# Optimization experiments

Hardware: AMD Instinct MI355X
Metric: run time of the kernel (lower is better)

## Reference

```python
import jax, jax.numpy as jnp
import numpy as np

RES = 8  # lattice resolution per dim (hardcoded in module)


def _neighbors():
    # 8 corner offsets of the unit cube, shape [8, 3]
    return jnp.stack(jnp.meshgrid(*([jnp.arange(2)] * 3), indexing='ij'), axis=-1).reshape(8, 3)


def _conv3d_periodic(img, kernel):
    # img: [D, H, W, Cin]; kernel: [3, 3, 3, Cout, Cin] (DHWOI layout, as in the module)
    x = jnp.pad(img, ((1, 1), (1, 1), (1, 1), (0, 0)), mode='wrap')[None]  # periodic box
    out = jax.lax.conv_general_dilated(
        x, kernel, window_strides=(1, 1, 1), padding='VALID',
        dimension_numbers=('NDHWC', 'DHWOI', 'NDHWC'))
    return out[0]


def setup_inputs() -> dict:
    key = jax.random.key(0)
    k1, k2, k3, k4, k5 = jax.random.split(key, 5)
    N, CIN, COUT, CHID = 500000, 32, 32, 32
    pos = jax.random.uniform(k1, (N, 3), dtype=jnp.float32)          # positions in [0,1)
    inp = jax.random.normal(k2, (N, CIN), dtype=jnp.float32)          # per-point features
    encoder_kernel = jax.random.normal(k3, (3, 3, 3, CHID, CIN), dtype=jnp.float32)
    inner_kernel = jax.random.normal(k4, (1, 3, 3, 3, CHID, CHID), dtype=jnp.float32)
    decoder_kernel = jax.random.normal(k5, (3, 3, 3, COUT, CHID), dtype=jnp.float32)
    return {"pos": pos, "input": inp, "encoder_kernel": encoder_kernel,
            "inner_kernel": inner_kernel, "decoder_kernel": decoder_kernel}


def reference(pos, input, encoder_kernel, inner_kernel, decoder_kernel):
    res = RES
    offsets = _neighbors()                                   # [8, 3]
    scaled = pos * res                                       # [N, 3]
    base = jnp.floor(scaled)
    frac = scaled - base                                     # trilinear fractions in [0,1)
    idxs = (base.astype(jnp.int32)[:, None, :] + offsets[None]) % res   # [N, 8, 3]
    # trilinear weights: prod over dims of frac (corner=1) or 1-frac (corner=0)
    w = jnp.where(offsets[None].astype(frac.dtype) == 1.0,
                  frac[:, None, :], 1.0 - frac[:, None, :])  # [N, 8, 3]
    weights = jnp.prod(w, axis=-1)                           # [N, 8]

    # scatter-add point features into the 8x8x8 lattice
    C = input.shape[-1]
    img = jnp.zeros((res, res, res, C), input.dtype).at[
        idxs[..., 0], idxs[..., 1], idxs[..., 2]].add(weights[..., None] * input[:, None, :])

    out = _conv3d_periodic(img, encoder_kernel)
    for k in inner_kernel:                                   # num_inner=1 residual silu blocks
        r = out
        out = r + jax.nn.silu(_conv3d_periodic(r, k))
    out = _conv3d_periodic(out, decoder_kernel)

    # gather back at the 8 corner cells (AggregationMethod.Nothing), then sum corners
    gathered = out[idxs[..., 0], idxs[..., 1], idxs[..., 2]]  # [N, 8, Cout]
    return gathered.sum(axis=1).reshape(input.shape[0], -1)
```

## Files before the change

### kernel.cpp

```cpp
#include <hip/hip_runtime.h>
#include <hip/hip_bf16.h>
#include <math.h>

#define NCELL 512
#define IMG_F 16384
#define NB    256
#define SPLIT 4

__global__ __launch_bounds__(256) void k_hist(
    const float* __restrict__ pos, int n, int* __restrict__ blockCnt)
{
    __shared__ int h[NCELL];
    const int t = threadIdx.x;
    for (int i = t; i < NCELL; i += 256) h[i] = 0;
    __syncthreads();
    const int stride = NB * 256;
    for (int p = blockIdx.x * 256 + t; p < n; p += stride) {
        const int ix = ((int)floorf(pos[3*p+0]*8.f)) & 7;
        const int iy = ((int)floorf(pos[3*p+1]*8.f)) & 7;
        const int iz = ((int)floorf(pos[3*p+2]*8.f)) & 7;
        atomicAdd(&h[ix*64 + iy*8 + iz], 1);
    }
    __syncthreads();
    for (int i = t; i < NCELL; i += 256)
        blockCnt[i * NB + blockIdx.x] = h[i];
}

__global__ __launch_bounds__(NB) void k_colscan(
    const int* __restrict__ blockCnt,
    int* __restrict__ relBase,
    int* __restrict__ cellTot)
{
    __shared__ int s[NB];
    const int cell = blockIdx.x, b = threadIdx.x;
    const int v = blockCnt[cell * NB + b];
    s[b] = v;
    __syncthreads();
    int acc = v;
    for (int off = 1; off < NB; off <<= 1) {
        const int add = (b >= off) ? s[b - off] : 0;
        __syncthreads();
        acc += add;
        s[b] = acc;
        __syncthreads();
    }
    relBase[cell * NB + b] = acc - v;
    if (b == NB - 1) cellTot[cell] = acc;
}

__global__ __launch_bounds__(NCELL) void k_scan512(
    const int* __restrict__ cellTot, int* __restrict__ binStart)
{
    __shared__ int s[NCELL];
    const int t = threadIdx.x;
    const int v = cellTot[t];
    s[t] = v;
    __syncthreads();
    int acc = v;
    for (int off = 1; off < NCELL; off <<= 1) {
        const int add = (t >= off) ? s[t - off] : 0;
        __syncthreads();
        acc += add;
        s[t] = acc;
        __syncthreads();
    }
    binStart[t] = acc - v;
    if (t == NCELL - 1) binStart[NCELL] = acc;
}

__global__ __launch_bounds__(256) void k_reorder(
    const float* __restrict__ pos, int n,
    const int* __restrict__ relBase, const int* __restrict__ binStart,
    float4* __restrict__ meta)
{
    __shared__ int cur[NCELL];
    const int t = threadIdx.x;
    for (int i = t; i < NCELL; i += 256)
        cur[i] = binStart[i] + relBase[i * NB + blockIdx.x];
    __syncthreads();
    const int stride = NB * 256;
    for (int p = blockIdx.x * 256 + t; p < n; p += stride) {
        const float sx = pos[3*p+0]*8.f, sy = pos[3*p+1]*8.f, sz = pos[3*p+2]*8.f;
        const float bx = floorf(sx), by = floorf(sy), bz = floorf(sz);
        const int ix = ((int)bx) & 7, iy = ((int)by) & 7, iz = ((int)bz) & 7;
        const int cell = ix*64 + iy*8 + iz;
        const int slot = atomicAdd(&cur[cell], 1);
        meta[slot] = make_float4(sx - bx, sy - by, sz - bz, __int_as_float(p));
    }
}

__global__ __launch_bounds__(512, 8) void k_accum(
    const float4* __restrict__ meta,
    const float* __restrict__ feat,
    const int* __restrict__ binStart,
    float* __restrict__ Mbuf)
{
    const int cell  = blockIdx.x >> 2;
    const int split = blockIdx.x & (SPLIT - 1);
    const int t = threadIdx.x;
    const int c = t & 31, sub = t >> 5;
    const int b0 = binStart[cell], cnt = binStart[cell + 1] - b0;
    const int s0 = b0 + (cnt * split) / SPLIT;
    const int s1 = b0 + (cnt * (split + 1)) / SPLIT;

    float acc[8];
    #pragma unroll
    for (int k = 0; k < 8; k++) acc[k] = 0.f;

    int i = s0 + sub;
    for (; i + 48 < s1; i += 64) {
        float4 m[4];
        float  v[4];
        #pragma unroll
        for (int j = 0; j < 4; j++) m[j] = meta[i + 16*j];
        #pragma unroll
        for (int j = 0; j < 4; j++)
            v[j] = feat[(size_t)__float_as_int(m[j].w) * 32 + c];
        #pragma unroll
        for (int j = 0; j < 4; j++) {
            const float gx = 1.f - m[j].x, gy = 1.f - m[j].y, gz = 1.f - m[j].z;
            const float a00 = gx*gy, a01 = gx*m[j].y, a10 = m[j].x*gy, a11 = m[j].x*m[j].y;
            acc[0] = fmaf(a00 * gz,     v[j], acc[0]);
            acc[1] = fmaf(a00 * m[j].z, v[j], acc[1]);
            acc[2] = fmaf(a01 * gz,     v[j], acc[2]);
            acc[3] = fmaf(a01 * m[j].z, v[j], acc[3]);
            acc[4] = fmaf(a10 * gz,     v[j], acc[4]);
            acc[5] = fmaf(a10 * m[j].z, v[j], acc[5]);
            acc[6] = fmaf(a11 * gz,     v[j], acc[6]);
            acc[7] = fmaf(a11 * m[j].z, v[j], acc[7]);
        }
    }
    for (; i < s1; i += 16) {
        const float4 m = meta[i];
        const float v = feat[(size_t)__float_as_int(m.w) * 32 + c];
        const float gx = 1.f - m.x, gy = 1.f - m.y, gz = 1.f - m.z;
        const float a00 = gx*gy, a01 = gx*m.y, a10 = m.x*gy, a11 = m.x*m.y;
        acc[0] = fmaf(a00 * gz,  v, acc[0]);
        acc[1] = fmaf(a00 * m.z, v, acc[1]);
        acc[2] = fmaf(a01 * gz,  v, acc[2]);
        acc[3] = fmaf(a01 * m.z, v, acc[3]);
        acc[4] = fmaf(a10 * gz,  v, acc[4]);
        acc[5] = fmaf(a10 * m.z, v, acc[5]);
        acc[6] = fmaf(a11 * gz,  v, acc[6]);
        acc[7] = fmaf(a11 * m.z, v, acc[7]);
    }

    __shared__ float red[16 * 8 * 32];
    #pragma unroll
    for (int k = 0; k < 8; k++) red[sub*256 + k*32 + c] = acc[k];
    __syncthreads();
    if (t < 256) {
        const int k = t >> 5, cc = t & 31;
        float s = 0.f;
        #pragma unroll
        for (int ss = 0; ss < 16; ss++) s += red[ss*256 + k*32 + cc];
        Mbuf[(blockIdx.x*8 + k)*32 + cc] = s;
    }
}

__global__ __launch_bounds__(256) void k_flush(
    const float* __restrict__ Mbuf, float* __restrict__ img)
{
    const int tid = blockIdx.x*256 + threadIdx.x;
    if (tid >= 4096) return;
    const int cell = tid >> 3, c4 = tid & 7;
    const int x = cell >> 6, y = (cell >> 3) & 7, z = cell & 7;
    const float4* M4 = (const float4*)Mbuf;
    float4 s = {0.f, 0.f, 0.f, 0.f};
    #pragma unroll
    for (int k = 0; k < 8; k++) {
        const int dx = (k >> 2) & 1, dy = (k >> 1) & 1, dz = k & 1;
        const int b = ((x - dx) & 7)*64 + ((y - dy) & 7)*8 + ((z - dz) & 7);
        #pragma unroll
        for (int sp = 0; sp < SPLIT; sp++) {
            const float4 v = M4[((b*SPLIT + sp)*8 + k)*8 + c4];
            s.x += v.x; s.y += v.y; s.z += v.z; s.w += v.w;
        }
    }
    ((float4*)img)[tid] = s;
}

template<int ACT>
__global__ __launch_bounds__(512) void k_conv(
    const float* __restrict__ in_lat,
    const float* __restrict__ w,
    float* __restrict__ out_lat)
{
    __shared__ float lds[72*36];
    __shared__ float red2[8*64];
    const int t = threadIdx.x;
    const int ixy = blockIdx.x >> 2;
    const int qq  = blockIdx.x & 3;
    const int ix = ixy >> 3, iy = ixy & 7;

    for (int i = t; i < 576; i += 512) {
        const int cellL = i >> 3, c4 = i & 7;
        const int s9 = cellL >> 3, nz = cellL & 7;
        const int jx = s9 / 3, jy = s9 - jx*3;
        const int gx = (ix + jx + 7) & 7, gy = (iy + jy + 7) & 7;
        const float4 v = ((const float4*)in_lat)[(gx*64 + gy*8 + nz)*8 + c4];
        *(float4*)&lds[cellL*36 + c4*4] = v;
    }
    __syncthreads();

    const int iz   = t & 7;
    const int co8  = (t >> 3) & 7;
    const int part = t >> 6;
    const int cout = qq*8 + co8;

    float4 acc = {0.f,0.f,0.f,0.f};
    const int tau0 = (part * 27) >> 3, tau1 = ((part + 1) * 27) >> 3;
    for (int tau = tau0; tau < tau1; ++tau) {
        const int kd = tau / 9, r = tau - kd*9;
        const int kh = r / 3,  kw = r - kh*3;
        const int nz = (iz + kw + 7) & 7;
        const float* lrow = &lds[((kd*3 + kh)*8 + nz)*36];
        const float* wrow = &w[(size_t)(tau*32 + cout)*32];
        #pragma unroll
        for (int c4i = 0; c4i < 8; c4i++) {
            const float4 a = *(const float4*)(lrow + c4i*4);
            const float4 b = *(const float4*)(wrow + c4i*4);
            acc.x = fmaf(a.x, b.x, acc.x);
            acc.y = fmaf(a.y, b.y, acc.y);
            acc.z = fmaf(a.z, b.z, acc.z);
            acc.w = fmaf(a.w, b.w, acc.w);
        }
    }
    red2[part*64 + co8*8 + iz] = (acc.x + acc.y) + (acc.z + acc.w);
    __syncthreads();

    if (t < 64) {
        const int oco8 = t >> 3, oiz = t & 7;
        float s = 0.f;
        #pragma unroll
        for (int pp = 0; pp < 8; pp++) s += red2[pp*64 + t];
        const int oidx = (ix*64 + iy*8 + oiz)*32 + qq*8 + oco8;
        if (ACT == 1) {
            const float rres = in_lat[oidx];
            s = rres + s / (1.f + expf(-s));
        }
        out_lat[oidx] = s;
    }
}

__global__ __launch_bounds__(256) void k_agg(
    const float* __restrict__ out_lat, float* __restrict__ agg)
{
    const int tid = blockIdx.x*256 + threadIdx.x;
    if (tid >= 4096) return;
    const int cell = tid >> 3, c4 = tid & 7;
    const int ix = cell >> 6, iy = (cell >> 3) & 7, iz = cell & 7;
    float4 s = {0.f,0.f,0.f,0.f};
    #pragma unroll
    for (int k = 0; k < 8; k++) {
        const int nx = (ix + ((k>>2)&1)) & 7;
        const int ny = (iy + ((k>>1)&1)) & 7;
        const int nz = (iz + (k&1)) & 7;
        const float4 v = ((const float4*)out_lat)[(nx*64 + ny*8 + nz)*8 + c4];
        s.x += v.x; s.y += v.y; s.z += v.z; s.w += v.w;
    }
    ((float4*)agg)[tid] = s;
}

__global__ __launch_bounds__(256) void k_gather(
    const float* __restrict__ pos,
    const float* __restrict__ agg,
    float* __restrict__ out,
    int n)
{
    const int tid = blockIdx.x*256 + threadIdx.x;
    const int p = tid >> 3, c4 = tid & 7;
    if (p >= n) return;
    const int ix = ((int)floorf(pos[3*p+0]*8.f)) & 7;
    const int iy = ((int)floorf(pos[3*p+1]*8.f)) & 7;
    const int iz = ((int)floorf(pos[3*p+2]*8.f)) & 7;
    ((float4*)out)[tid] = ((const float4*)agg)[(ix*64 + iy*8 + iz)*8 + c4];
}

extern "C" void kernel_launch(void* const* d_in, const int* in_sizes, int n_in,
                              void* d_out, int out_size, void* d_ws, size_t ws_size,
                              hipStream_t stream)
{
    const float* pos  = (const float*)d_in[0];
    const float* feat = (const float*)d_in[1];
    const float* wenc = (const float*)d_in[2];
    const float* winn = (const float*)d_in[3];
    const float* wdec = (const float*)d_in[4];
    float* out = (float*)d_out;
    const int n = in_sizes[0] / 3;

    float4* meta     = (float4*)d_ws;
    float*  Mbuf     = (float*)(meta + n);
    float*  img      = Mbuf + NCELL*SPLIT*8*32;
    float*  h1       = img  + IMG_F;
    float*  h2       = h1   + IMG_F;
    float*  olat     = h2   + IMG_F;
    float*  aggb     = olat + IMG_F;
    int*    blockCnt = (int*)(aggb + IMG_F);
    int*    relBase  = blockCnt + NCELL*NB;
    int*    cellTot  = relBase + NCELL*NB;
    int*    binStart = cellTot + NCELL;

    k_hist   <<<NB,    256, 0, stream>>>(pos, n, blockCnt);
    k_colscan<<<NCELL, NB,  0, stream>>>(blockCnt, relBase, cellTot);
    k_scan512<<<1,   NCELL, 0, stream>>>(cellTot, binStart);
    k_reorder<<<NB,    256, 0, stream>>>(pos, n, relBase, binStart, meta);
    k_accum  <<<NCELL*SPLIT, 512, 0, stream>>>(meta, feat, binStart, Mbuf);
    k_flush  <<<16,    256, 0, stream>>>(Mbuf, img);
    k_conv<0><<<256,   512, 0, stream>>>(img, wenc, h1);
    k_conv<1><<<256,   512, 0, stream>>>(h1,  winn, h2);
    k_conv<0><<<256,   512, 0, stream>>>(h2,  wdec, olat);
    k_agg    <<<16,    256, 0, stream>>>(olat, aggb);
    const int gblocks = (n*8 + 255)/256;
    k_gather <<<gblocks, 256, 0, stream>>>(pos, aggb, out, n);
}
```

Baseline: 177.6 us.

## Fold scan into reorder, flush into encoder conv, cache cell index for gather

The single-block 512-cell scan is merged into k_reorder: every block redundantly scans cellTot and block 0 writes binStart. The flush of the split accumulation buffer is fused into the encoder convolution's LDS fill, which removes the img buffer and one launch. k_reorder also stores a 16-bit cell index per point, so k_gather reads 2 bytes instead of 12 bytes of positions and skips the floor math. The trade-off is redundant scan work in every block, redundant flush reads in each conv block, and an extra 1 MB write in reorder.

```diff
diff --git a/kernel.cpp b/kernel.cpp
--- a/kernel.cpp
+++ b/kernel.cpp
@@ -48,44 +48,50 @@
     if (b == NB - 1) cellTot[cell] = acc;
 }
 
-__global__ __launch_bounds__(NCELL) void k_scan512(
-    const int* __restrict__ cellTot, int* __restrict__ binStart)
-{
-    __shared__ int s[NCELL];
-    const int t = threadIdx.x;
-    const int v = cellTot[t];
-    s[t] = v;
-    __syncthreads();
-    int acc = v;
-    for (int off = 1; off < NCELL; off <<= 1) {
-        const int add = (t >= off) ? s[t - off] : 0;
+__global__ __launch_bounds__(256) void k_reorder(
+    const float* __restrict__ pos, int n,
+    const int* __restrict__ relBase, const int* __restrict__ cellTot,
+    int* __restrict__ binStart,
+    float4* __restrict__ meta,
+    unsigned short* __restrict__ cellIdx)
+{
+    __shared__ int sScan[256];
+    __shared__ int cur[NCELL];
+    const int t = threadIdx.x;
+    const int bx = blockIdx.x;
+
+    const int v0 = cellTot[2*t], v1 = cellTot[2*t + 1];
+    const int ps = v0 + v1;
+    sScan[t] = ps;
+    __syncthreads();
+    int acc = ps;
+    for (int off = 1; off < 256; off <<= 1) {
+        const int add = (t >= off) ? sScan[t - off] : 0;
         __syncthreads();
         acc += add;
-        s[t] = acc;
+        sScan[t] = acc;
         __syncthreads();
     }
-    binStart[t] = acc - v;
-    if (t == NCELL - 1) binStart[NCELL] = acc;
-}
-
-__global__ __launch_bounds__(256) void k_reorder(
-    const float* __restrict__ pos, int n,
-    const int* __restrict__ relBase, const int* __restrict__ binStart,
-    float4* __restrict__ meta)
-{
-    __shared__ int cur[NCELL];
-    const int t = threadIdx.x;
-    for (int i = t; i < NCELL; i += 256)
-        cur[i] = binStart[i] + relBase[i * NB + blockIdx.x];
-    __syncthreads();
+    const int exclPair = acc - ps;
+    const int e0 = exclPair, e1 = exclPair + v0;
+    if (bx == 0) {
+        binStart[2*t]     = e0;
+        binStart[2*t + 1] = e1;
+        if (t == 255) binStart[NCELL] = acc;
+    }
+    cur[2*t]     = e0 + relBase[(2*t)     * NB + bx];
+    cur[2*t + 1] = e1 + relBase[(2*t + 1) * NB + bx];
+    __syncthreads();
+
     const int stride = NB * 256;
-    for (int p = blockIdx.x * 256 + t; p < n; p += stride) {
+    for (int p = bx * 256 + t; p < n; p += stride) {
         const float sx = pos[3*p+0]*8.f, sy = pos[3*p+1]*8.f, sz = pos[3*p+2]*8.f;
-        const float bx = floorf(sx), by = floorf(sy), bz = floorf(sz);
-        const int ix = ((int)bx) & 7, iy = ((int)by) & 7, iz = ((int)bz) & 7;
+        const float bxf = floorf(sx), byf = floorf(sy), bzf = floorf(sz);
+        const int ix = ((int)bxf) & 7, iy = ((int)byf) & 7, iz = ((int)bzf) & 7;
         const int cell = ix*64 + iy*8 + iz;
         const int slot = atomicAdd(&cur[cell], 1);
-        meta[slot] = make_float4(sx - bx, sy - by, sz - bz, __int_as_float(p));
+        meta[slot] = make_float4(sx - bxf, sy - byf, sz - bzf, __int_as_float(p));
+        cellIdx[p] = (unsigned short)cell;
     }
 }
 
@@ -158,26 +164,72 @@
     }
 }
 
-__global__ __launch_bounds__(256) void k_flush(
-    const float* __restrict__ Mbuf, float* __restrict__ img)
-{
-    const int tid = blockIdx.x*256 + threadIdx.x;
-    if (tid >= 4096) return;
-    const int cell = tid >> 3, c4 = tid & 7;
-    const int x = cell >> 6, y = (cell >> 3) & 7, z = cell & 7;
+__global__ __launch_bounds__(512) void k_conv_enc(
+    const float* __restrict__ Mbuf,
+    const float* __restrict__ w,
+    float* __restrict__ out_lat)
+{
+    __shared__ float lds[72*36];
+    __shared__ float red2[8*64];
+    const int t = threadIdx.x;
+    const int ixy = blockIdx.x >> 2;
+    const int qq  = blockIdx.x & 3;
+    const int ix = ixy >> 3, iy = ixy & 7;
     const float4* M4 = (const float4*)Mbuf;
-    float4 s = {0.f, 0.f, 0.f, 0.f};
-    #pragma unroll
-    for (int k = 0; k < 8; k++) {
-        const int dx = (k >> 2) & 1, dy = (k >> 1) & 1, dz = k & 1;
-        const int b = ((x - dx) & 7)*64 + ((y - dy) & 7)*8 + ((z - dz) & 7);
-        #pragma unroll
-        for (int sp = 0; sp < SPLIT; sp++) {
-            const float4 v = M4[((b*SPLIT + sp)*8 + k)*8 + c4];
-            s.x += v.x; s.y += v.y; s.z += v.z; s.w += v.w;
-        }
-    }
-    ((float4*)img)[tid] = s;
+
+    for (int i = t; i < 576; i += 512) {
+        const int cellL = i >> 3, c4 = i & 7;
+        const int s9 = cellL >> 3, nz = cellL & 7;
+        const int jx = s9 / 3, jy = s9 - jx*3;
+        const int gx = (ix + jx + 7) & 7, gy = (iy + jy + 7) & 7;
+        float4 s = {0.f,0.f,0.f,0.f};
+        #pragma unroll
+        for (int k = 0; k < 8; k++) {
+            const int dx = (k >> 2) & 1, dy = (k >> 1) & 1, dz = k & 1;
+            const int b = ((gx - dx) & 7)*64 + ((gy - dy) & 7)*8 + ((nz - dz) & 7);
+            #pragma unroll
+            for (int sp = 0; sp < SPLIT; sp++) {
+                const float4 v = M4[((b*SPLIT + sp)*8 + k)*8 + c4];
+                s.x += v.x; s.y += v.y; s.z += v.z; s.w += v.w;
+            }
+        }
+        *(float4*)&lds[cellL*36 + c4*4] = s;
+    }
+    __syncthreads();
+
+    const int iz   = t & 7;
+    const int co8  = (t >> 3) & 7;
+    const int part = t >> 6;
+    const int cout = qq*8 + co8;
+
+    float4 acc = {0.f,0.f,0.f,0.f};
+    const int tau0 = (part * 27) >> 3, tau1 = ((part + 1) * 27) >> 3;
+    for (int tau = tau0; tau < tau1; ++tau) {
+        const int kd = tau / 9, r = tau - kd*9;
+        const int kh = r / 3,  kw = r - kh*3;
+        const int nz = (iz + kw + 7) & 7;
+        const float* lrow = &lds[((kd*3 + kh)*8 + nz)*36];
+        const float* wrow = &w[(size_t)(tau*32 + cout)*32];
+        #pragma unroll
+        for (int c4i = 0; c4i < 8; c4i++) {
+            const float4 a = *(const float4*)(lrow + c4i*4);
+            const float4 b = *(const float4*)(wrow + c4i*4);
+            acc.x = fmaf(a.x, b.x, acc.x);
+            acc.y = fmaf(a.y, b.y, acc.y);
+            acc.z = fmaf(a.z, b.z, acc.z);
+            acc.w = fmaf(a.w, b.w, acc.w);
+        }
+    }
+    red2[part*64 + co8*8 + iz] = (acc.x + acc.y) + (acc.z + acc.w);
+    __syncthreads();
+
+    if (t < 64) {
+        const int oco8 = t >> 3, oiz = t & 7;
+        float s = 0.f;
+        #pragma unroll
+        for (int pp = 0; pp < 8; pp++) s += red2[pp*64 + t];
+        out_lat[(ix*64 + iy*8 + oiz)*32 + qq*8 + oco8] = s;
+    }
 }
 
 template<int ACT>
@@ -263,7 +315,7 @@
 }
 
 __global__ __launch_bounds__(256) void k_gather(
-    const float* __restrict__ pos,
+    const unsigned short* __restrict__ cellIdx,
     const float* __restrict__ agg,
     float* __restrict__ out,
     int n)
@@ -271,10 +323,8 @@
     const int tid = blockIdx.x*256 + threadIdx.x;
     const int p = tid >> 3, c4 = tid & 7;
     if (p >= n) return;
-    const int ix = ((int)floorf(pos[3*p+0]*8.f)) & 7;
-    const int iy = ((int)floorf(pos[3*p+1]*8.f)) & 7;
-    const int iz = ((int)floorf(pos[3*p+2]*8.f)) & 7;
-    ((float4*)out)[tid] = ((const float4*)agg)[(ix*64 + iy*8 + iz)*8 + c4];
+    const int cell = cellIdx[p];
+    ((float4*)out)[tid] = ((const float4*)agg)[cell*8 + c4];
 }
 
 extern "C" void kernel_launch(void* const* d_in, const int* in_sizes, int n_in,
@@ -291,8 +341,7 @@
 
     float4* meta     = (float4*)d_ws;
     float*  Mbuf     = (float*)(meta + n);
-    float*  img      = Mbuf + NCELL*SPLIT*8*32;
-    float*  h1       = img  + IMG_F;
+    float*  h1       = Mbuf + NCELL*SPLIT*8*32;
     float*  h2       = h1   + IMG_F;
     float*  olat     = h2   + IMG_F;
     float*  aggb     = olat + IMG_F;
@@ -300,17 +349,17 @@
     int*    relBase  = blockCnt + NCELL*NB;
     int*    cellTot  = relBase + NCELL*NB;
     int*    binStart = cellTot + NCELL;
-
-    k_hist   <<<NB,    256, 0, stream>>>(pos, n, blockCnt);
-    k_colscan<<<NCELL, NB,  0, stream>>>(blockCnt, relBase, cellTot);
-    k_scan512<<<1,   NCELL, 0, stream>>>(cellTot, binStart);
-    k_reorder<<<NB,    256, 0, stream>>>(pos, n, relBase, binStart, meta);
-    k_accum  <<<NCELL*SPLIT, 512, 0, stream>>>(meta, feat, binStart, Mbuf);
-    k_flush  <<<16,    256, 0, stream>>>(Mbuf, img);
-    k_conv<0><<<256,   512, 0, stream>>>(img, wenc, h1);
-    k_conv<1><<<256,   512, 0, stream>>>(h1,  winn, h2);
-    k_conv<0><<<256,   512, 0, stream>>>(h2,  wdec, olat);
-    k_agg    <<<16,    256, 0, stream>>>(olat, aggb);
+    unsigned short* cellIdx = (unsigned short*)(binStart + NCELL + 3);
+
+    k_hist    <<<NB,    256, 0, stream>>>(pos, n, blockCnt);
+    k_colscan <<<NCELL, NB,  0, stream>>>(blockCnt, relBase, cellTot);
+    k_reorder <<<NB,    256, 0, stream>>>(pos, n, relBase, cellTot, binStart,
+                                          meta, cellIdx);
+    k_accum   <<<NCELL*SPLIT, 512, 0, stream>>>(meta, feat, binStart, Mbuf);
+    k_conv_enc<<<256,   512, 0, stream>>>(Mbuf, wenc, h1);
+    k_conv<1> <<<256,   512, 0, stream>>>(h1,  winn, h2);
+    k_conv<0> <<<256,   512, 0, stream>>>(h2,  wdec, olat);
+    k_agg     <<<16,    256, 0, stream>>>(olat, aggb);
     const int gblocks = (n*8 + 255)/256;
-    k_gather <<<gblocks, 256, 0, stream>>>(pos, aggb, out, n);
-}
+    k_gather  <<<gblocks, 256, 0, stream>>>(cellIdx, aggb, out, n);
+}
```

Result: no change. 177.6 us (-0.0%).
